# Kernel tuning notes

Measured on AMD Instinct MI355X. Metric: run time of the kernel, lower is better.

## Reference

```python
import jax, jax.numpy as jnp
import numpy as np

B, N, F_IN, F_OUT = 4, 4096, 300, 300


def setup_inputs() -> dict:
    key = jax.random.key(0)
    k1, k2, k3, k4 = jax.random.split(key, 4)
    text = jax.random.normal(k1, (B, N, F_IN), dtype=jnp.float32)
    adj = jax.random.uniform(k2, (B, N, N), dtype=jnp.float32)
    # parameters (the torch module leaves them uninitialized; use small random)
    weight = jax.random.normal(k3, (F_IN, F_OUT), dtype=jnp.float32) * (1.0 / np.sqrt(F_IN))
    bias = jax.random.normal(k4, (F_OUT,), dtype=jnp.float32) * 0.01
    return {"text": text, "adj": adj, "weight": weight, "bias": bias}


def reference(text, adj, weight, bias):
    # denom = rowsum(adj) + 1; D = diag(denom^-0.5) per batch
    # D @ adj @ D  ==  adj * d_i * d_j  (broadcast scaling, no dense diagonals)
    denom = jnp.sum(adj, axis=2) + 1.0            # [B, N]
    d = denom ** -0.5                              # [B, N]
    norm_adj = adj * d[:, :, None] * d[:, None, :]  # [B, N, N]
    # (norm_adj @ text) @ weight, contracted efficiently
    agg = jnp.matmul(norm_adj, text)               # [B, N, F_in]
    out = jnp.matmul(agg, weight) + bias           # [B, N, F_out]
    return out
```

## Files before the change

### kernel.cpp

```cpp
#include <hip/hip_runtime.h>
#include <hip/hip_bf16.h>

typedef __bf16 bf16x8 __attribute__((ext_vector_type(8)));
typedef __bf16 bf16x4 __attribute__((ext_vector_type(4)));
typedef float  f32x4  __attribute__((ext_vector_type(4)));

#define B_   4
#define N_   4096
#define FIN  300
#define FOUT 300
#define FP   320
#define MT   64
#define KT   64
#define NMT  (N_/MT)
#define NKT  (N_/KT)
#define TILE_BYTES (MT*KT*2)
#define STEP_BYTES 18432
#define YTILE 2048

#define WT_OFF   0
#define D_OFF    (512*1024)
#define TSC_OFF  (1024*1024)
#define YT_OFF   (16*1024*1024)
#define ADJB_OFF (32*1024*1024)
#define ADJB_BYTES ((size_t)B_ * N_ * N_ * 2)

#define SB() __builtin_amdgcn_sched_barrier(0)

__device__ __forceinline__ void gload_lds16(const void* g, void* l) {
    __builtin_amdgcn_global_load_lds((const __attribute__((address_space(1))) void*)g,
                                     (__attribute__((address_space(3))) void*)l, 16, 0, 0);
}

__global__ void k_wt(const float* __restrict__ W, __bf16* __restrict__ Wt) {
    int t = blockIdx.x * 256 + threadIdx.x;
    if (t >= FP * FP) return;
    int f = t / FP, k = t - f * FP;
    float v = (f < FOUT && k < FIN) ? W[k * FOUT + f] : 0.0f;
    Wt[t] = (__bf16)v;
}

__global__ void k_rowsum(const float* __restrict__ adj, float* __restrict__ d) {
    int row  = blockIdx.x * 4 + (threadIdx.x >> 6);
    int lane = threadIdx.x & 63;
    const float4* p = (const float4*)(adj + (size_t)row * N_);
    float s = 0.0f;
#pragma unroll
    for (int it = 0; it < 16; ++it) {
        float4 v = p[it * 64 + lane];
        s += v.x + v.y + v.z + v.w;
    }
#pragma unroll
    for (int off = 32; off; off >>= 1) s += __shfl_xor(s, off);
    if (lane == 0) d[row] = rsqrtf(s + 1.0f);
}

__global__ __launch_bounds__(512) void k_rowsum_cvt(const float* __restrict__ adj,
                                                    float* __restrict__ d,
                                                    char* __restrict__ adjb) {
    __shared__ __align__(16) char lds[4 * TILE_BYTES];
    const int mt = blockIdx.x, b = blockIdx.y;
    const int t = threadIdx.x, w = t >> 6, lane = t & 63;
    const int tloc = lane >> 4;
    const int chunk = (lane & 15) >> 1;
    const int sub8  = (lane & 1) * 8;
    const size_t rowbase = (size_t)b * N_ + mt * 64;
    char* gbase = adjb + (size_t)((b * NMT + mt) * NKT) * TILE_BYTES;

    float psum[8] = {};
    for (int g = 0; g < 16; ++g) {
#pragma unroll
        for (int rr = 0; rr < 8; ++rr) {
            int r = w * 8 + rr;
            float4 v = *(const float4*)(adj + (rowbase + r) * N_ + g * 256 + lane * 4);
            psum[rr] += v.x + v.y + v.z + v.w;
            bf16x4 o;
            o[0] = (__bf16)v.x; o[1] = (__bf16)v.y; o[2] = (__bf16)v.z; o[3] = (__bf16)v.w;
            int byte = tloc * TILE_BYTES + r * 128 + ((chunk * 16) ^ ((r & 7) << 4)) + sub8;
            *(bf16x4*)(lds + byte) = o;
        }
        __syncthreads();
#pragma unroll
        for (int i = 0; i < 4; ++i) {
            int idx = i * 512 + t;
            int tl = idx >> 9, off = (idx & 511) * 16;
            *(f32x4*)(gbase + (size_t)(g * 4 + tl) * TILE_BYTES + off) =
                *(const f32x4*)(lds + tl * TILE_BYTES + off);
        }
        __syncthreads();
    }
#pragma unroll
    for (int rr = 0; rr < 8; ++rr) {
        float s = psum[rr];
#pragma unroll
        for (int off = 32; off; off >>= 1) s += __shfl_xor(s, off);
        if (lane == 0) d[rowbase + w * 8 + rr] = rsqrtf(s + 1.0f);
    }
}

__global__ void k_tsc(const float* __restrict__ text, const float* __restrict__ d,
                      __bf16* __restrict__ Tsc) {
    int t = blockIdx.x * 256 + threadIdx.x;
    int j = t / FP;
    int k = t - j * FP;
    float v = 0.0f;
    if (k < FIN) v = d[j] * text[(size_t)j * FIN + k];
    Tsc[t] = (__bf16)v;
}

__global__ __launch_bounds__(256) void k_y(const __bf16* __restrict__ Wt,
                                           const __bf16* __restrict__ Tsc,
                                           __bf16* __restrict__ Yt) {
    int b    = blockIdx.y;
    int j0   = blockIdx.x * 64;
    int wave = threadIdx.x >> 6, lane = threadIdx.x & 63;
    int lr = lane & 15, lg = lane >> 4;
    f32x4 acc[5][4] = {};
    for (int k0 = 0; k0 < FP; k0 += 32) {
        bf16x8 a[5], bb[4];
#pragma unroll
        for (int fi = 0; fi < 5; ++fi) {
            int f = (wave * 5 + fi) * 16 + lr;
            a[fi] = *(const bf16x8*)(Wt + (size_t)f * FP + k0 + lg * 8);
        }
#pragma unroll
        for (int ji = 0; ji < 4; ++ji) {
            int j = j0 + ji * 16 + lr;
            bb[ji] = *(const bf16x8*)(Tsc + ((size_t)(b * N_ + j)) * FP + k0 + lg * 8);
        }
#pragma unroll
        for (int fi = 0; fi < 5; ++fi)
#pragma unroll
            for (int ji = 0; ji < 4; ++ji)
                acc[fi][ji] = __builtin_amdgcn_mfma_f32_16x16x32_bf16(a[fi], bb[ji], acc[fi][ji], 0, 0, 0);
    }
#pragma unroll
    for (int fi = 0; fi < 5; ++fi)
#pragma unroll
        for (int ji = 0; ji < 4; ++ji)
#pragma unroll
            for (int r = 0; r < 4; ++r) {
                int f = (wave * 5 + fi) * 16 + lg * 4 + r;
                int j = j0 + ji * 16 + lr;
                Yt[((size_t)b * FP + f) * N_ + j] = (__bf16)acc[fi][ji][r];
            }
}

__global__ __launch_bounds__(256) void k_y_t(const __bf16* __restrict__ Wt,
                                             const __bf16* __restrict__ Tsc,
                                             char* __restrict__ Ytt) {
    int b    = blockIdx.y;
    int j0   = blockIdx.x * 64;
    int wave = threadIdx.x >> 6, lane = threadIdx.x & 63;
    int lr = lane & 15, lg = lane >> 4;
    f32x4 acc[5][4] = {};
    for (int k0 = 0; k0 < FP; k0 += 32) {
        bf16x8 a[5], bb[4];
#pragma unroll
        for (int fi = 0; fi < 5; ++fi) {
            int f = (wave * 5 + fi) * 16 + lr;
            a[fi] = *(const bf16x8*)(Wt + (size_t)f * FP + k0 + lg * 8);
        }
#pragma unroll
        for (int ji = 0; ji < 4; ++ji) {
            int j = j0 + ji * 16 + lr;
            bb[ji] = *(const bf16x8*)(Tsc + ((size_t)(b * N_ + j)) * FP + k0 + lg * 8);
        }
#pragma unroll
        for (int fi = 0; fi < 5; ++fi)
#pragma unroll
            for (int ji = 0; ji < 4; ++ji)
                acc[fi][ji] = __builtin_amdgcn_mfma_f32_16x16x32_bf16(a[fi], bb[ji], acc[fi][ji], 0, 0, 0);
    }
#pragma unroll
    for (int fi = 0; fi < 5; ++fi)
#pragma unroll
        for (int ji = 0; ji < 4; ++ji)
#pragma unroll
            for (int r = 0; r < 4; ++r) {
                int f = (wave * 5 + fi) * 16 + lg * 4 + r;
                int j = j0 + ji * 16 + lr;
                int ft = f >> 4, floc = f & 15;
                int kt = j >> 6, jloc = j & 63;
                size_t base = (size_t)((b * 20 + ft) * 64 + kt) * YTILE;
                int byte = floc * 128 + (((jloc >> 3) * 16) ^ ((floc & 7) << 4)) + (jloc & 7) * 2;
                *(__bf16*)(Ytt + base + byte) = (__bf16)acc[fi][ji][r];
            }
}

__global__ __launch_bounds__(256) void k_gemm_pipe(const char* __restrict__ adjb,
                                                   const char* __restrict__ ytt,
                                                   const float* __restrict__ d,
                                                   const float* __restrict__ bias,
                                                   float* __restrict__ out) {
    __shared__ __align__(16) char smem[3 * STEP_BYTES];
    const int bid = blockIdx.x;
    const int bx = bid & 63, by = (bid >> 6) & 3, b = bid >> 8;
    const int w = threadIdx.x >> 6, lane = threadIdx.x & 63;
    const int lr = lane & 15, lg = lane >> 4;

    const char* gp[5];
    int st[5];
    int lo[5];
#pragma unroll
    for (int g = 0; g < 5; ++g) {
        int cid = w * 5 + g; if (cid >= 18) cid -= 18;
        if (cid < 8) {
            gp[g] = adjb + (size_t)((b * NMT + bx) * NKT) * TILE_BYTES + cid * 1024 + lane * 16;
            st[g] = TILE_BYTES;
            lo[g] = cid * 1024;
        } else {
            int cc = cid - 8;
            gp[g] = ytt + (size_t)((b * 20 + by * 5 + (cc >> 1)) * 64) * YTILE + (cc & 1) * 1024 + lane * 16;
            st[g] = YTILE;
            lo[g] = 8192 + cc * 1024;
        }
    }

    uint32_t sb = (uint32_t)(uintptr_t)(__attribute__((address_space(3))) char*)smem;
    const int sw = (lr & 7) << 4;
    const uint32_t col0 = (uint32_t)((lg * 16) ^ sw);
    const uint32_t col1 = (uint32_t)(((4 + lg) * 16) ^ sw);
    const uint32_t rowA = sb + (w * 16 + lr) * 128;
    uint32_t rowB[5];
#pragma unroll
    for (int nt = 0; nt < 5; ++nt) rowB[nt] = sb + 8192 + nt * YTILE + lr * 128;

    f32x4 acc[5] = {};
    uint32_t oc = 0, on = STEP_BYTES, ot = 2 * STEP_BYTES;

#define STAGE(OFF, KT_) { _Pragma("unroll") \
    for (int g = 0; g < 5; ++g) \
        gload_lds16(gp[g] + (size_t)(KT_) * st[g], smem + (OFF) + lo[g]); }

    STAGE(oc, 0)
    STAGE(on, 1)
    for (int t = 0; t < NKT; ++t) {
        int ks = t + 2 > NKT - 1 ? NKT - 1 : t + 2;
        SB();
        STAGE(ot, ks)
        SB();
        asm volatile("s_waitcnt vmcnt(10)");
        SB();
        __builtin_amdgcn_s_barrier();
        bf16x8 a0, a1, b00, b01, b10, b11, b20, b21, b30, b31, b40, b41;
        asm volatile("ds_read_b128 %0, %1" : "=v"(a0)  : "v"(oc + rowA + col0));
        asm volatile("ds_read_b128 %0, %1" : "=v"(a1)  : "v"(oc + rowA + col1));
        asm volatile("ds_read_b128 %0, %1" : "=v"(b00) : "v"(oc + rowB[0] + col0));
        asm volatile("ds_read_b128 %0, %1" : "=v"(b01) : "v"(oc + rowB[0] + col1));
        asm volatile("ds_read_b128 %0, %1" : "=v"(b10) : "v"(oc + rowB[1] + col0));
        asm volatile("ds_read_b128 %0, %1" : "=v"(b11) : "v"(oc + rowB[1] + col1));
        asm volatile("ds_read_b128 %0, %1" : "=v"(b20) : "v"(oc + rowB[2] + col0));
        asm volatile("ds_read_b128 %0, %1" : "=v"(b21) : "v"(oc + rowB[2] + col1));
        asm volatile("ds_read_b128 %0, %1" : "=v"(b30) : "v"(oc + rowB[3] + col0));
        asm volatile("ds_read_b128 %0, %1" : "=v"(b31) : "v"(oc + rowB[3] + col1));
        asm volatile("ds_read_b128 %0, %1" : "=v"(b40) : "v"(oc + rowB[4] + col0));
        asm volatile("ds_read_b128 %0, %1" : "=v"(b41) : "v"(oc + rowB[4] + col1));
        asm volatile("s_waitcnt lgkmcnt(0)");
        SB();
        __builtin_amdgcn_s_barrier();
        acc[0] = __builtin_amdgcn_mfma_f32_16x16x32_bf16(a0, b00, acc[0], 0, 0, 0);
        acc[0] = __builtin_amdgcn_mfma_f32_16x16x32_bf16(a1, b01, acc[0], 0, 0, 0);
        acc[1] = __builtin_amdgcn_mfma_f32_16x16x32_bf16(a0, b10, acc[1], 0, 0, 0);
        acc[1] = __builtin_amdgcn_mfma_f32_16x16x32_bf16(a1, b11, acc[1], 0, 0, 0);
        acc[2] = __builtin_amdgcn_mfma_f32_16x16x32_bf16(a0, b20, acc[2], 0, 0, 0);
        acc[2] = __builtin_amdgcn_mfma_f32_16x16x32_bf16(a1, b21, acc[2], 0, 0, 0);
        acc[3] = __builtin_amdgcn_mfma_f32_16x16x32_bf16(a0, b30, acc[3], 0, 0, 0);
        acc[3] = __builtin_amdgcn_mfma_f32_16x16x32_bf16(a1, b31, acc[3], 0, 0, 0);
        acc[4] = __builtin_amdgcn_mfma_f32_16x16x32_bf16(a0, b40, acc[4], 0, 0, 0);
        acc[4] = __builtin_amdgcn_mfma_f32_16x16x32_bf16(a1, b41, acc[4], 0, 0, 0);
        SB();
        uint32_t tmp = oc; oc = on; on = ot; ot = tmp;
    }

    const int rowb = bx * 64 + w * 16;
    float di[4];
#pragma unroll
    for (int r = 0; r < 4; ++r)
        di[r] = d[b * N_ + rowb + lg * 4 + r];
#pragma unroll
    for (int nt = 0; nt < 5; ++nt) {
        int f = by * 80 + nt * 16 + lr;
        if (f < FOUT) {
            float bv = bias[f];
#pragma unroll
            for (int r = 0; r < 4; ++r) {
                int i = rowb + lg * 4 + r;
                out[((size_t)b * N_ + i) * FOUT + f] = di[r] * acc[nt][r] + bv;
            }
        }
    }
#undef STAGE
}

#define FB_LOAD(AV, BV, K0)                                                           \
    {                                                                                 \
        _Pragma("unroll")                                                             \
        for (int mi = 0; mi < 2; ++mi) {                                              \
            const float4* p = (const float4*)(adjf + (size_t)(rowbase + mi * 16 + lr) * N_ + (K0) + lg * 8); \
            float4 v0 = p[0], v1 = p[1];                                              \
            AV[mi][0] = (__bf16)v0.x; AV[mi][1] = (__bf16)v0.y;                       \
            AV[mi][2] = (__bf16)v0.z; AV[mi][3] = (__bf16)v0.w;                       \
            AV[mi][4] = (__bf16)v1.x; AV[mi][5] = (__bf16)v1.y;                       \
            AV[mi][6] = (__bf16)v1.z; AV[mi][7] = (__bf16)v1.w;                       \
        }                                                                             \
        _Pragma("unroll")                                                             \
        for (int nt = 0; nt < 10; ++nt) {                                             \
            int f = wn * 160 + nt * 16 + lr;                                          \
            BV[nt] = *(const bf16x8*)(Yb + (size_t)f * N_ + (K0) + lg * 8);           \
        }                                                                             \
    }
#define FB_MFMA(AV, BV)                                                               \
    {                                                                                 \
        _Pragma("unroll")                                                             \
        for (int mi = 0; mi < 2; ++mi)                                                \
            _Pragma("unroll")                                                         \
            for (int nt = 0; nt < 10; ++nt)                                           \
                acc[mi][nt] = __builtin_amdgcn_mfma_f32_16x16x32_bf16(AV[mi], BV[nt], acc[mi][nt], 0, 0, 0); \
    }

__global__ __launch_bounds__(256) void k_gemm_fb(const float* __restrict__ adj,
                                                 const __bf16* __restrict__ Yt,
                                                 const float* __restrict__ d,
                                                 const float* __restrict__ bias,
                                                 float* __restrict__ out) {
    int b    = blockIdx.y;
    int wave = threadIdx.x >> 6, lane = threadIdx.x & 63;
    int wm = wave & 1, wn = wave >> 1;
    int lr = lane & 15, lg = lane >> 4;
    int rowbase = blockIdx.x * 64 + wm * 32;
    const float*  adjf = adj + (size_t)b * N_ * N_;
    const __bf16* Yb   = Yt + (size_t)b * FP * N_;

    f32x4 acc[2][10] = {};
    bf16x8 aA[2], bA[10], aB[2], bB[10];

    FB_LOAD(aA, bA, 0)
    for (int k0 = 0; k0 < N_ - 64; k0 += 64) {
        FB_LOAD(aB, bB, k0 + 32)
        FB_MFMA(aA, bA)
        FB_LOAD(aA, bA, k0 + 64)
        FB_MFMA(aB, bB)
    }
    FB_LOAD(aB, bB, N_ - 32)
    FB_MFMA(aA, bA)
    FB_MFMA(aB, bB)

#pragma unroll
    for (int mi = 0; mi < 2; ++mi) {
        float di[4];
#pragma unroll
        for (int r = 0; r < 4; ++r)
            di[r] = d[b * N_ + rowbase + mi * 16 + lg * 4 + r];
#pragma unroll
        for (int nt = 0; nt < 10; ++nt) {
            int f = wn * 160 + nt * 16 + lr;
            if (f < FOUT) {
                float bv = bias[f];
#pragma unroll
                for (int r = 0; r < 4; ++r) {
                    int i = rowbase + mi * 16 + lg * 4 + r;
                    out[((size_t)b * N_ + i) * FOUT + f] = di[r] * acc[mi][nt][r] + bv;
                }
            }
        }
    }
}

extern "C" void kernel_launch(void* const* d_in, const int* in_sizes, int n_in,
                              void* d_out, int out_size, void* d_ws, size_t ws_size,
                              hipStream_t stream) {
    const float* text = (const float*)d_in[0];
    const float* adj  = (const float*)d_in[1];
    const float* W    = (const float*)d_in[2];
    const float* bias = (const float*)d_in[3];
    float* out = (float*)d_out;

    char* ws = (char*)d_ws;
    __bf16* Wt   = (__bf16*)(ws + WT_OFF);
    float*  dv   = (float*)(ws + D_OFF);
    __bf16* Tsc  = (__bf16*)(ws + TSC_OFF);
    char*   Ybuf = ws + YT_OFF;
    char*   adjb = ws + ADJB_OFF;

    bool big = ws_size >= (size_t)ADJB_OFF + ADJB_BYTES;

    k_wt<<<dim3((FP * FP + 255) / 256), dim3(256), 0, stream>>>(W, Wt);
    if (big)
        k_rowsum_cvt<<<dim3(NMT, B_), dim3(512), 0, stream>>>(adj, dv, adjb);
    else
        k_rowsum<<<dim3(B_ * N_ / 4), dim3(256), 0, stream>>>(adj, dv);
    k_tsc<<<dim3(B_ * N_ * FP / 256), dim3(256), 0, stream>>>(text, dv, Tsc);
    if (big) {
        k_y_t<<<dim3(N_ / 64, B_), dim3(256), 0, stream>>>(Wt, Tsc, Ybuf);
        k_gemm_pipe<<<dim3(1024), dim3(256), 0, stream>>>(adjb, Ybuf, dv, bias, out);
    } else {
        k_y<<<dim3(N_ / 64, B_), dim3(256), 0, stream>>>(Wt, Tsc, (__bf16*)Ybuf);
        k_gemm_fb<<<dim3(N_ / 64, B_), dim3(256), 0, stream>>>(adj, (__bf16*)Ybuf, dv, bias, out);
    }
}
```

Measured before the change: 203.6 us.

## Enlarge GEMM block tile to 128x80 with 2 waves each owning 64 rows

Restructures the main adj·Y GEMM so each block computes 128 rows × 80 columns with two waves, each wave owning a 4×5 grid of MFMA accumulators instead of a 1×5 strip. This raises MFMA-to-LDS-read ratio and halves the Y-tile reloads per output row, cutting LDS and global traffic per flop. Block order is changed so batch/row tiles iterate fastest, and setprio is added around the MFMA burst. The cost is fewer waves per block, a 512-block grid, more registers and larger LDS staging, which may reduce occupancy and latency hiding.

Measured after the change: 193.7 us. 4.9% less time.

```diff
diff --git a/kernel.cpp b/kernel.cpp
--- a/kernel.cpp
+++ b/kernel.cpp
@@ -15,8 +15,8 @@
 #define NMT  (N_/MT)
 #define NKT  (N_/KT)
 #define TILE_BYTES (MT*KT*2)
-#define STEP_BYTES 18432
 #define YTILE 2048
+#define STEP_B2 26624
 
 #define WT_OFF   0
 #define D_OFF    (512*1024)
@@ -188,32 +188,35 @@
             }
 }
 
-__global__ __launch_bounds__(256) void k_gemm_pipe(const char* __restrict__ adjb,
+__global__ __launch_bounds__(128) void k_gemm_pipe(const char* __restrict__ adjb,
                                                    const char* __restrict__ ytt,
                                                    const float* __restrict__ d,
                                                    const float* __restrict__ bias,
                                                    float* __restrict__ out) {
-    __shared__ __align__(16) char smem[3 * STEP_BYTES];
+    __shared__ __align__(16) char smem[3 * STEP_B2];
     const int bid = blockIdx.x;
-    const int bx = bid & 63, by = (bid >> 6) & 3, b = bid >> 8;
+    const int bx  = bid & 31;
+    const int b   = (bid >> 5) & 3;
+    const int by  = bid >> 7;
     const int w = threadIdx.x >> 6, lane = threadIdx.x & 63;
     const int lr = lane & 15, lg = lane >> 4;
 
-    const char* gp[5];
-    int st[5];
-    int lo[5];
-#pragma unroll
-    for (int g = 0; g < 5; ++g) {
-        int cid = w * 5 + g; if (cid >= 18) cid -= 18;
-        if (cid < 8) {
-            gp[g] = adjb + (size_t)((b * NMT + bx) * NKT) * TILE_BYTES + cid * 1024 + lane * 16;
+    const char* gp[13];
+    int st[13], lo[13];
+#pragma unroll
+    for (int g = 0; g < 13; ++g) {
+        int cid = w * 13 + g;
+        if (cid < 16) {
+            gp[g] = adjb + (size_t)((b * NMT + bx * 2 + (cid >> 3)) * NKT) * TILE_BYTES
+                    + (cid & 7) * 1024 + lane * 16;
             st[g] = TILE_BYTES;
             lo[g] = cid * 1024;
         } else {
-            int cc = cid - 8;
-            gp[g] = ytt + (size_t)((b * 20 + by * 5 + (cc >> 1)) * 64) * YTILE + (cc & 1) * 1024 + lane * 16;
+            int cc = cid - 16;
+            gp[g] = ytt + (size_t)((b * 20 + by * 5 + (cc >> 1)) * 64) * YTILE
+                    + (cc & 1) * 1024 + lane * 16;
             st[g] = YTILE;
-            lo[g] = 8192 + cc * 1024;
+            lo[g] = 16384 + cc * 1024;
         }
     }
 
@@ -221,76 +224,79 @@
     const int sw = (lr & 7) << 4;
     const uint32_t col0 = (uint32_t)((lg * 16) ^ sw);
     const uint32_t col1 = (uint32_t)(((4 + lg) * 16) ^ sw);
-    const uint32_t rowA = sb + (w * 16 + lr) * 128;
+    uint32_t rowA[4];
+#pragma unroll
+    for (int mi = 0; mi < 4; ++mi)
+        rowA[mi] = sb + w * 8192 + (mi * 16 + lr) * 128;
     uint32_t rowB[5];
 #pragma unroll
-    for (int nt = 0; nt < 5; ++nt) rowB[nt] = sb + 8192 + nt * YTILE + lr * 128;
-
-    f32x4 acc[5] = {};
-    uint32_t oc = 0, on = STEP_BYTES, ot = 2 * STEP_BYTES;
-
-#define STAGE(OFF, KT_) { _Pragma("unroll") \
-    for (int g = 0; g < 5; ++g) \
-        gload_lds16(gp[g] + (size_t)(KT_) * st[g], smem + (OFF) + lo[g]); }
-
-    STAGE(oc, 0)
-    STAGE(on, 1)
+    for (int nt = 0; nt < 5; ++nt) rowB[nt] = sb + 16384 + nt * YTILE + lr * 128;
+
+    f32x4 acc[4][5] = {};
+    uint32_t oc = 0, on = STEP_B2, ot = 2 * STEP_B2;
+
+#pragma unroll
+    for (int g = 0; g < 13; ++g) gload_lds16(gp[g], smem + lo[g]);
+#pragma unroll
+    for (int g = 0; g < 13; ++g) gload_lds16(gp[g] + st[g], smem + STEP_B2 + lo[g]);
+
     for (int t = 0; t < NKT; ++t) {
         int ks = t + 2 > NKT - 1 ? NKT - 1 : t + 2;
         SB();
-        STAGE(ot, ks)
+#pragma unroll
+        for (int g = 0; g < 13; ++g)
+            gload_lds16(gp[g] + (size_t)ks * st[g], smem + ot + lo[g]);
         SB();
-        asm volatile("s_waitcnt vmcnt(10)");
+        asm volatile("s_waitcnt vmcnt(26)");
         SB();
         __builtin_amdgcn_s_barrier();
-        bf16x8 a0, a1, b00, b01, b10, b11, b20, b21, b30, b31, b40, b41;
-        asm volatile("ds_read_b128 %0, %1" : "=v"(a0)  : "v"(oc + rowA + col0));
-        asm volatile("ds_read_b128 %0, %1" : "=v"(a1)  : "v"(oc + rowA + col1));
-        asm volatile("ds_read_b128 %0, %1" : "=v"(b00) : "v"(oc + rowB[0] + col0));
-        asm volatile("ds_read_b128 %0, %1" : "=v"(b01) : "v"(oc + rowB[0] + col1));
-        asm volatile("ds_read_b128 %0, %1" : "=v"(b10) : "v"(oc + rowB[1] + col0));
-        asm volatile("ds_read_b128 %0, %1" : "=v"(b11) : "v"(oc + rowB[1] + col1));
-        asm volatile("ds_read_b128 %0, %1" : "=v"(b20) : "v"(oc + rowB[2] + col0));
-        asm volatile("ds_read_b128 %0, %1" : "=v"(b21) : "v"(oc + rowB[2] + col1));
-        asm volatile("ds_read_b128 %0, %1" : "=v"(b30) : "v"(oc + rowB[3] + col0));
-        asm volatile("ds_read_b128 %0, %1" : "=v"(b31) : "v"(oc + rowB[3] + col1));
-        asm volatile("ds_read_b128 %0, %1" : "=v"(b40) : "v"(oc + rowB[4] + col0));
-        asm volatile("ds_read_b128 %0, %1" : "=v"(b41) : "v"(oc + rowB[4] + col1));
+        bf16x8 af[4][2], bf[5][2];
+#pragma unroll
+        for (int mi = 0; mi < 4; ++mi) {
+            asm volatile("ds_read_b128 %0, %1" : "=v"(af[mi][0]) : "v"(oc + rowA[mi] + col0));
+            asm volatile("ds_read_b128 %0, %1" : "=v"(af[mi][1]) : "v"(oc + rowA[mi] + col1));
+        }
+#pragma unroll
+        for (int nt = 0; nt < 5; ++nt) {
+            asm volatile("ds_read_b128 %0, %1" : "=v"(bf[nt][0]) : "v"(oc + rowB[nt] + col0));
+            asm volatile("ds_read_b128 %0, %1" : "=v"(bf[nt][1]) : "v"(oc + rowB[nt] + col1));
+        }
         asm volatile("s_waitcnt lgkmcnt(0)");
         SB();
         __builtin_amdgcn_s_barrier();
-        acc[0] = __builtin_amdgcn_mfma_f32_16x16x32_bf16(a0, b00, acc[0], 0, 0, 0);
-        acc[0] = __builtin_amdgcn_mfma_f32_16x16x32_bf16(a1, b01, acc[0], 0, 0, 0);
-        acc[1] = __builtin_amdgcn_mfma_f32_16x16x32_bf16(a0, b10, acc[1], 0, 0, 0);
-        acc[1] = __builtin_amdgcn_mfma_f32_16x16x32_bf16(a1, b11, acc[1], 0, 0, 0);
-        acc[2] = __builtin_amdgcn_mfma_f32_16x16x32_bf16(a0, b20, acc[2], 0, 0, 0);
-        acc[2] = __builtin_amdgcn_mfma_f32_16x16x32_bf16(a1, b21, acc[2], 0, 0, 0);
-        acc[3] = __builtin_amdgcn_mfma_f32_16x16x32_bf16(a0, b30, acc[3], 0, 0, 0);
-        acc[3] = __builtin_amdgcn_mfma_f32_16x16x32_bf16(a1, b31, acc[3], 0, 0, 0);
-        acc[4] = __builtin_amdgcn_mfma_f32_16x16x32_bf16(a0, b40, acc[4], 0, 0, 0);
-        acc[4] = __builtin_amdgcn_mfma_f32_16x16x32_bf16(a1, b41, acc[4], 0, 0, 0);
+        __builtin_amdgcn_s_setprio(1);
+#pragma unroll
+        for (int kh = 0; kh < 2; ++kh)
+#pragma unroll
+            for (int mi = 0; mi < 4; ++mi)
+#pragma unroll
+                for (int nt = 0; nt < 5; ++nt)
+                    acc[mi][nt] = __builtin_amdgcn_mfma_f32_16x16x32_bf16(af[mi][kh], bf[nt][kh], acc[mi][nt], 0, 0, 0);
+        __builtin_amdgcn_s_setprio(0);
         SB();
         uint32_t tmp = oc; oc = on; on = ot; ot = tmp;
     }
 
-    const int rowb = bx * 64 + w * 16;
-    float di[4];
-#pragma unroll
-    for (int r = 0; r < 4; ++r)
-        di[r] = d[b * N_ + rowb + lg * 4 + r];
-#pragma unroll
-    for (int nt = 0; nt < 5; ++nt) {
-        int f = by * 80 + nt * 16 + lr;
-        if (f < FOUT) {
-            float bv = bias[f];
-#pragma unroll
-            for (int r = 0; r < 4; ++r) {
-                int i = rowb + lg * 4 + r;
-                out[((size_t)b * N_ + i) * FOUT + f] = di[r] * acc[nt][r] + bv;
+    const int rowb = bx * 128 + w * 64;
+#pragma unroll
+    for (int mi = 0; mi < 4; ++mi) {
+        float di[4];
+#pragma unroll
+        for (int r = 0; r < 4; ++r)
+            di[r] = d[b * N_ + rowb + mi * 16 + lg * 4 + r];
+#pragma unroll
+        for (int nt = 0; nt < 5; ++nt) {
+            int f = by * 80 + nt * 16 + lr;
+            if (f < FOUT) {
+                float bv = bias[f];
+#pragma unroll
+                for (int r = 0; r < 4; ++r) {
+                    int i = rowb + mi * 16 + lg * 4 + r;
+                    out[((size_t)b * N_ + i) * FOUT + f] = di[r] * acc[mi][nt][r] + bv;
+                }
             }
         }
     }
-#undef STAGE
 }
 
 #define FB_LOAD(AV, BV, K0)                                                           \
@@ -393,7 +399,7 @@
     k_tsc<<<dim3(B_ * N_ * FP / 256), dim3(256), 0, stream>>>(text, dv, Tsc);
     if (big) {
         k_y_t<<<dim3(N_ / 64, B_), dim3(256), 0, stream>>>(Wt, Tsc, Ybuf);
-        k_gemm_pipe<<<dim3(1024), dim3(256), 0, stream>>>(adjb, Ybuf, dv, bias, out);
+        k_gemm_pipe<<<dim3(512), dim3(128), 0, stream>>>(adjb, Ybuf, dv, bias, out);
     } else {
         k_y<<<dim3(N_ / 64, B_), dim3(256), 0, stream>>>(Wt, Tsc, (__bf16*)Ybuf);
         k_gemm_fb<<<dim3(N_ / 64, B_), dim3(256), 0, stream>>>(adj, (__bf16*)Ybuf, dv, bias, out);
```
